# Kernel optimization log

Hardware: AMD Instinct MI355X
Metric: run time of the kernel (lower is better)

## Reference

```python
import jax, jax.numpy as jnp
import numpy as np

N = 100000
E = 1600000
IN_C, HID_C, OUT_C = 128, 128, 64


def setup_inputs() -> dict:
    key = jax.random.key(0)
    k1, k2, k3, k4 = jax.random.split(key, 4)
    x = jax.random.normal(k1, (N, IN_C), dtype=jnp.float32)
    edge_index = jax.random.randint(k2, (2, E), 0, N, dtype=jnp.int32)
    # Glorot-ish scaled weights
    W1 = jax.random.normal(k3, (IN_C, HID_C), dtype=jnp.float32) / np.sqrt(IN_C)
    b1 = jnp.zeros((HID_C,), dtype=jnp.float32)
    W2 = jax.random.normal(k4, (HID_C, OUT_C), dtype=jnp.float32) / np.sqrt(HID_C)
    b2 = jnp.zeros((OUT_C,), dtype=jnp.float32)
    return {"x": x, "edge_index": edge_index, "W1": W1, "b1": b1, "W2": W2, "b2": b2}


def _gcn_norm(edge_index, num_nodes):
    """Add self loops and compute symmetric D^{-1/2} A D^{-1/2} edge weights (PyG GCNConv defaults)."""
    loop = jnp.arange(num_nodes, dtype=edge_index.dtype)
    row = jnp.concatenate([edge_index[0], loop])  # source nodes
    col = jnp.concatenate([edge_index[1], loop])  # target nodes
    ones = jnp.ones_like(col, dtype=jnp.float32)
    deg = jax.ops.segment_sum(ones, col, num_segments=num_nodes)
    deg_inv_sqrt = jnp.where(deg > 0, jax.lax.rsqrt(jnp.maximum(deg, 1.0)), 0.0)
    norm = deg_inv_sqrt[row] * deg_inv_sqrt[col]  # [E+N]
    return row, col, norm


def _gcn_layer(x, row, col, norm, W, b, num_nodes):
    h = x @ W                                   # [N, C_out] transform first (PyG order)
    msg = h[row] * norm[:, None]                # gather + scale  [E+N, C_out]
    out = jax.ops.segment_sum(msg, col, num_segments=num_nodes)  # scatter-add
    return out + b


def reference(x, edge_index, W1, b1, W2, b2):
    row, col, norm = _gcn_norm(edge_index, N)
    h = jax.nn.relu(_gcn_layer(x, row, col, norm, W1, b1, N))
    return _gcn_layer(h, row, col, norm, W2, b2, N)
```

## Files before the change

### kernel.cpp

```cpp
#include <hip/hip_runtime.h>
#include <hip/hip_fp16.h>

#define NODES 100000
#define EDGES 1600000

#define BSHIFT 9
#define BNODES 512
#define NBUCK ((NODES + BNODES - 1) / BNODES)
#define BCAP 10240

#define GB 782
#define SC 1563

typedef __attribute__((ext_vector_type(8))) short short8;
typedef __attribute__((ext_vector_type(4))) float f32x4;

__device__ inline unsigned short f2bf(float f) {
    unsigned u = __builtin_bit_cast(unsigned, f);
    u = u + 0x7fff + ((u >> 16) & 1);
    return (unsigned short)(u >> 16);
}
__device__ inline float bf2f(unsigned short h) {
    unsigned u = ((unsigned)h) << 16;
    return __builtin_bit_cast(float, u);
}
__device__ inline unsigned short f2h_bits(float f) {
    __half h = __float2half_rn(f);
    return __builtin_bit_cast(unsigned short, h);
}
__device__ inline float h2f(unsigned short bits) {
    return __half2float(__builtin_bit_cast(__half, bits));
}
__device__ inline float2 h2f2(unsigned int bits) {
    __half2 h = __builtin_bit_cast(__half2, bits);
    return __half22float2(h);
}


template <int NCOL>
__device__ __forceinline__ void w_frag_prep(const float* __restrict__ W,
                                            unsigned short* __restrict__ wh,
                                            unsigned short* __restrict__ wl,
                                            int idx) {
    constexpr int NCT = NCOL / 16;
    int lane = idx & 63;
    int rem = idx >> 6;
    int ct = rem % NCT;
    int kt = rem / NCT;
    int kbase = kt * 32 + ((lane >> 4) * 8);
    int c = ct * 16 + (lane & 15);
#pragma unroll
    for (int i = 0; i < 8; i++) {
        float v = W[(size_t)(kbase + i) * NCOL + c];
        unsigned short hi = f2bf(v);
        unsigned short lo = f2bf(v - bf2f(hi));
        wh[(size_t)idx * 8 + i] = hi;
        wl[(size_t)idx * 8 + i] = lo;
    }
}

__global__ __launch_bounds__(256) void prep_kernel(const float* __restrict__ W1,
                                                   const float* __restrict__ W2,
                                                   unsigned short* __restrict__ wh1,
                                                   unsigned short* __restrict__ wl1,
                                                   unsigned short* __restrict__ wh2,
                                                   unsigned short* __restrict__ wl2,
                                                   int* __restrict__ gcur) {
    const int tid = threadIdx.x;
    const int b = blockIdx.x;
    if (b < 8) {
        w_frag_prep<128>(W1, wh1, wl1, b * 256 + tid);
    } else if (b < 12) {
        w_frag_prep<64>(W2, wh2, wl2, (b - 8) * 256 + tid);
    } else {
        if (tid < NBUCK) gcur[tid] = 0;
    }
}


template <int NCOL, bool IN_HALF>
__device__ __forceinline__ void gemm_body(const void* __restrict__ Xv,
                                          const unsigned short* __restrict__ wh,
                                          const unsigned short* __restrict__ wl,
                                          unsigned short* __restrict__ H,
                                          unsigned short* s_wh,
                                          unsigned short* s_wl,
                                          int tid, int bid) {
    constexpr int NCT = NCOL / 16;
    constexpr int FRAGS = 4 * NCT * 64;

    const int wave = tid >> 6;
    const int lane = tid & 63;

    const int row0 = bid * 128 + wave * 16 + (lane & 15);
    const bool active = (bid * 128 + wave * 16) < NODES;

    float xs[4][8];
    if (active) {
        if constexpr (IN_HALF) {
            const unsigned short* xrow = (const unsigned short*)Xv + (size_t)row0 * 128 + ((lane >> 4) * 8);
#pragma unroll
            for (int kt = 0; kt < 4; kt++) {
                short8 raw = *(const short8*)(xrow + kt * 32);
#pragma unroll
                for (int i = 0; i < 8; i++) xs[kt][i] = h2f((unsigned short)raw[i]);
            }
        } else {
            const float* xrow = (const float*)Xv + (size_t)row0 * 128 + ((lane >> 4) * 8);
#pragma unroll
            for (int kt = 0; kt < 4; kt++) {
                float4 a = *(const float4*)(xrow + kt * 32);
                float4 b = *(const float4*)(xrow + kt * 32 + 4);
                xs[kt][0] = a.x; xs[kt][1] = a.y; xs[kt][2] = a.z; xs[kt][3] = a.w;
                xs[kt][4] = b.x; xs[kt][5] = b.y; xs[kt][6] = b.z; xs[kt][7] = b.w;
            }
        }
    }

    constexpr int ROUNDS = (FRAGS * 16) / (512 * 16);
#pragma unroll
    for (int j = 0; j < ROUNDS; j++) {
        __builtin_amdgcn_global_load_lds((const unsigned int*)((const char*)wh + ((size_t)tid + j * 512) * 16),
                                         (unsigned int*)(s_wh + ((size_t)tid + j * 512) * 8), 16, 0, 0);
        __builtin_amdgcn_global_load_lds((const unsigned int*)((const char*)wl + ((size_t)tid + j * 512) * 16),
                                         (unsigned int*)(s_wl + ((size_t)tid + j * 512) * 8), 16, 0, 0);
    }
    __syncthreads();

    if (!active) return;

    short8 ah[4], al[4];
#pragma unroll
    for (int kt = 0; kt < 4; kt++) {
#pragma unroll
        for (int i = 0; i < 8; i++) {
            unsigned short hi = f2bf(xs[kt][i]);
            unsigned short lo = f2bf(xs[kt][i] - bf2f(hi));
            ah[kt][i] = (short)hi;
            al[kt][i] = (short)lo;
        }
    }

    f32x4 acc[NCT];
#pragma unroll
    for (int ct = 0; ct < NCT; ct++) acc[ct] = (f32x4){0.f, 0.f, 0.f, 0.f};

#pragma unroll
    for (int kt = 0; kt < 4; kt++) {
#pragma unroll
        for (int ct = 0; ct < NCT; ct++) {
            const int fo = ((kt * NCT + ct) * 64 + lane) * 8;
            short8 bh = *(const short8*)&s_wh[fo];
            short8 bl = *(const short8*)&s_wl[fo];
            acc[ct] = __builtin_amdgcn_mfma_f32_16x16x32_bf16(ah[kt], bh, acc[ct], 0, 0, 0);
            acc[ct] = __builtin_amdgcn_mfma_f32_16x16x32_bf16(al[kt], bh, acc[ct], 0, 0, 0);
            acc[ct] = __builtin_amdgcn_mfma_f32_16x16x32_bf16(ah[kt], bl, acc[ct], 0, 0, 0);
        }
    }

    const int rbase = bid * 128 + wave * 16 + ((lane >> 4) * 4);
#pragma unroll
    for (int ct = 0; ct < NCT; ct++) {
#pragma unroll
        for (int r = 0; r < 4; r++) {
            H[(size_t)(rbase + r) * NCOL + ct * 16 + (lane & 15)] = f2h_bits(acc[ct][r]);
        }
    }
}


__global__ __launch_bounds__(512) void gemm1_scatter(const float* __restrict__ X,
                                                     const unsigned short* __restrict__ wh,
                                                     const unsigned short* __restrict__ wl,
                                                     unsigned short* __restrict__ H,
                                                     const int* __restrict__ erow,
                                                     const int* __restrict__ ecol,
                                                     int* __restrict__ gcur,
                                                     int2* __restrict__ temp) {
    __shared__ __align__(16) char smem[65536];
    const int tid = threadIdx.x;

    if (blockIdx.x < GB) {
        unsigned short* s_wh = (unsigned short*)smem;
        unsigned short* s_wl = s_wh + 2048 * 8;
        gemm_body<128, false>(X, wh, wl, H, s_wh, s_wl, tid, blockIdx.x);
    } else {
        int* hist = (int*)smem;
        int* rbase = hist + NBUCK;
        const int ebase = (blockIdx.x - GB) * 1024;
        if (tid < NBUCK) hist[tid] = 0;
        __syncthreads();

        const int e0 = ebase + tid;
        const int e1 = ebase + tid + 512;
        const bool v0 = e0 < EDGES;
        const bool v1 = e1 < EDGES;
        int c0 = 0, s0 = 0, b0 = 0, r0 = 0;
        int c1 = 0, s1 = 0, b1 = 0, r1 = 0;
        if (v0) {
            c0 = ecol[e0]; s0 = erow[e0];
            b0 = c0 >> BSHIFT;
            r0 = atomicAdd(&hist[b0], 1);
        }
        if (v1) {
            c1 = ecol[e1]; s1 = erow[e1];
            b1 = c1 >> BSHIFT;
            r1 = atomicAdd(&hist[b1], 1);
        }
        __syncthreads();
        if (tid < NBUCK) {
            int h = hist[tid];
            rbase[tid] = h ? atomicAdd(&gcur[tid], h) : 0;
        }
        __syncthreads();
        if (v0) {
            int2 v; v.x = s0; v.y = c0 & (BNODES - 1);
            temp[(size_t)b0 * BCAP + rbase[b0] + r0] = v;
        }
        if (v1) {
            int2 v; v.x = s1; v.y = c1 & (BNODES - 1);
            temp[(size_t)b1 * BCAP + rbase[b1] + r1] = v;
        }
    }
}


__global__ __launch_bounds__(512) void gemm2_kernel(const unsigned short* __restrict__ X,
                                                    const unsigned short* __restrict__ wh,
                                                    const unsigned short* __restrict__ wl,
                                                    unsigned short* __restrict__ H) {
    __shared__ unsigned short s_wh[1024 * 8];
    __shared__ unsigned short s_wl[1024 * 8];
    gemm_body<64, true>(X, wh, wl, H, s_wh, s_wl, threadIdx.x, blockIdx.x);
}


__global__ __launch_bounds__(1024) void bucket_build(const int2* __restrict__ temp,
                                                     const int* __restrict__ gcur,
                                                     int* __restrict__ row_start,
                                                     float* __restrict__ dis,
                                                     int* __restrict__ esrc) {
    __shared__ int cnt[BNODES];
    __shared__ int offs[BNODES];
    __shared__ int cur[BNODES];
    __shared__ int ssc[256];
    const int b = blockIdx.x;
    const int tid = threadIdx.x;

    if (tid < 256) ssc[tid] = (tid < NBUCK) ? gcur[tid] : 0;
    __syncthreads();
    for (int d = 1; d < 256; d <<= 1) {
        int x = (tid < 256 && tid >= d) ? ssc[tid - d] : 0;
        __syncthreads();
        if (tid < 256) ssc[tid] += x;
        __syncthreads();
    }
    const int size = gcur[b];
    const int gbase = ssc[b] - size;
    if (b == 0 && tid == 0) row_start[NODES] = EDGES;

    if (tid < BNODES) cnt[tid] = 0;
    __syncthreads();

    for (int i = tid; i < size; i += 1024) {
        int2 v = temp[(size_t)b * BCAP + i];
        atomicAdd(&cnt[v.y], 1);
    }
    __syncthreads();

    if (tid < BNODES) offs[tid] = cnt[tid];
    __syncthreads();
    for (int d = 1; d < BNODES; d <<= 1) {
        int x = 0;
        if (tid < BNODES && tid >= d) x = offs[tid - d];
        __syncthreads();
        if (tid < BNODES) offs[tid] += x;
        __syncthreads();
    }
    if (tid < BNODES) {
        int excl = offs[tid] - cnt[tid];
        cur[tid] = excl;
        int v = b * BNODES + tid;
        if (v < NODES) {
            row_start[v] = gbase + excl;
            dis[v] = rsqrtf((float)(cnt[tid] + 1));
        }
    }
    __syncthreads();

    for (int i = tid; i < size; i += 1024) {
        int2 v = temp[(size_t)b * BCAP + i];
        int pos = gbase + atomicAdd(&cur[v.y], 1);
        esrc[pos] = v.x;
    }
}


template <int C, bool RELU, bool OUT_HALF>
__global__ __launch_bounds__(256, 8) void agg_v4(const unsigned short* __restrict__ H,
                                                 const int* __restrict__ row_start,
                                                 const int* __restrict__ edge_src,
                                                 const float* __restrict__ dis,
                                                 const float* __restrict__ bias,
                                                 void* __restrict__ OUT) {
    constexpr int GL = (C == 128) ? 16 : 8;
    constexpr int GPW = 64 / GL;
    constexpr int RQ = C / 8;

    const int lane = threadIdx.x & 63;
    const int sub = lane & (GL - 1);
    const int grp = lane >> ((C == 128) ? 4 : 3);
    const int wid = (blockIdx.x * 256 + threadIdx.x) >> 6;
    const int v = wid * GPW + grp;
    if (v >= NODES) return;

    const uint4* __restrict__ Hq = (const uint4*)H;

    const int e0 = row_start[v];
    const int e1 = row_start[v + 1];
    const float dv = dis[v];

    const float4 ba = ((const float4*)bias)[sub * 2];
    const float4 bb = ((const float4*)bias)[sub * 2 + 1];

    uint4 gs = Hq[(size_t)v * RQ + sub];

    int i0 = edge_src[min(e0 + 0, EDGES - 1)];
    int i1 = edge_src[min(e0 + 1, EDGES - 1)];
    int i2 = edge_src[min(e0 + 2, EDGES - 1)];
    int i3 = edge_src[min(e0 + 3, EDGES - 1)];
    float d0 = dis[i0], d1 = dis[i1], d2 = dis[i2], d3 = dis[i3];

    float a0, a1, a2, a3, a4, a5, a6, a7;
    {
        float2 f0 = h2f2(gs.x), f1 = h2f2(gs.y), f2 = h2f2(gs.z), f3 = h2f2(gs.w);
        a0 = f0.x * dv; a1 = f0.y * dv; a2 = f1.x * dv; a3 = f1.y * dv;
        a4 = f2.x * dv; a5 = f2.y * dv; a6 = f3.x * dv; a7 = f3.y * dv;
    }

    for (int k = e0; k < e1; k += 4) {
        uint4 g0 = Hq[(size_t)i0 * RQ + sub];
        uint4 g1 = Hq[(size_t)i1 * RQ + sub];
        uint4 g2 = Hq[(size_t)i2 * RQ + sub];
        uint4 g3 = Hq[(size_t)i3 * RQ + sub];
        const int n0 = edge_src[min(k + 4, EDGES - 1)];
        const int n1 = edge_src[min(k + 5, EDGES - 1)];
        const int n2 = edge_src[min(k + 6, EDGES - 1)];
        const int n3 = edge_src[min(k + 7, EDGES - 1)];
        const float dn0 = dis[n0], dn1 = dis[n1], dn2 = dis[n2], dn3 = dis[n3];
        const float w0 = d0;
        const float w1 = (k + 1 < e1) ? d1 : 0.f;
        const float w2 = (k + 2 < e1) ? d2 : 0.f;
        const float w3 = (k + 3 < e1) ? d3 : 0.f;
#define ACC(G, W)                                                        \
        {                                                                \
            float2 f0 = h2f2(G.x), f1 = h2f2(G.y);                       \
            float2 f2 = h2f2(G.z), f3 = h2f2(G.w);                       \
            a0 = fmaf(f0.x, W, a0); a1 = fmaf(f0.y, W, a1);              \
            a2 = fmaf(f1.x, W, a2); a3 = fmaf(f1.y, W, a3);              \
            a4 = fmaf(f2.x, W, a4); a5 = fmaf(f2.y, W, a5);              \
            a6 = fmaf(f3.x, W, a6); a7 = fmaf(f3.y, W, a7);              \
        }
        ACC(g0, w0)
        ACC(g1, w1)
        ACC(g2, w2)
        ACC(g3, w3)
#undef ACC
        i0 = n0; i1 = n1; i2 = n2; i3 = n3;
        d0 = dn0; d1 = dn1; d2 = dn2; d3 = dn3;
    }

    float o0 = fmaf(a0, dv, ba.x);
    float o1 = fmaf(a1, dv, ba.y);
    float o2 = fmaf(a2, dv, ba.z);
    float o3 = fmaf(a3, dv, ba.w);
    float o4 = fmaf(a4, dv, bb.x);
    float o5 = fmaf(a5, dv, bb.y);
    float o6 = fmaf(a6, dv, bb.z);
    float o7 = fmaf(a7, dv, bb.w);
    if constexpr (RELU) {
        o0 = fmaxf(o0, 0.f); o1 = fmaxf(o1, 0.f);
        o2 = fmaxf(o2, 0.f); o3 = fmaxf(o3, 0.f);
        o4 = fmaxf(o4, 0.f); o5 = fmaxf(o5, 0.f);
        o6 = fmaxf(o6, 0.f); o7 = fmaxf(o7, 0.f);
    }

    if constexpr (OUT_HALF) {
        uint4 o;
        o.x = __builtin_bit_cast(unsigned, __float22half2_rn(make_float2(o0, o1)));
        o.y = __builtin_bit_cast(unsigned, __float22half2_rn(make_float2(o2, o3)));
        o.z = __builtin_bit_cast(unsigned, __float22half2_rn(make_float2(o4, o5)));
        o.w = __builtin_bit_cast(unsigned, __float22half2_rn(make_float2(o6, o7)));
        ((uint4*)OUT)[(size_t)v * RQ + sub] = o;
    } else {
        float4 oa, ob;
        oa.x = o0; oa.y = o1; oa.z = o2; oa.w = o3;
        ob.x = o4; ob.y = o5; ob.z = o6; ob.w = o7;
        float* outp = (float*)OUT + (size_t)v * C + sub * 8;
        *(float4*)(outp) = oa;
        *(float4*)(outp + 4) = ob;
    }
}


extern "C" void kernel_launch(void* const* d_in, const int* in_sizes, int n_in,
                              void* d_out, int out_size, void* d_ws, size_t ws_size,
                              hipStream_t stream) {
    const float* x   = (const float*)d_in[0];
    const int* eidx  = (const int*)d_in[1];
    const float* W1  = (const float*)d_in[2];
    const float* b1  = (const float*)d_in[3];
    const float* W2  = (const float*)d_in[4];
    const float* b2  = (const float*)d_in[5];
    float* out = (float*)d_out;

    const int* erow = eidx;
    const int* ecol = eidx + EDGES;

    char* w = (char*)d_ws;
    size_t off = 0;
    auto alloc = [&](size_t bytes) -> void* {
        void* p = w + off;
        off += (bytes + 255) & ~(size_t)255;
        return p;
    };
    float* dis     = (float*)alloc((size_t)NODES * 4);
    int*   rowst   = (int*)alloc((size_t)(NODES + 1) * 4);
    int*   esrc    = (int*)alloc((size_t)EDGES * 4);
    int*   gcur    = (int*)alloc(NBUCK * 4);
    int2*  temp    = (int2*)alloc((size_t)NBUCK * BCAP * 8);
    unsigned short* wh1 = (unsigned short*)alloc(2048 * 8 * 2);
    unsigned short* wl1 = (unsigned short*)alloc(2048 * 8 * 2);
    unsigned short* wh2 = (unsigned short*)alloc(1024 * 8 * 2);
    unsigned short* wl2 = (unsigned short*)alloc(1024 * 8 * 2);
    unsigned short* bufA = (unsigned short*)alloc((size_t)NODES * 128 * 2);
    unsigned short* bufB = (unsigned short*)alloc((size_t)NODES * 128 * 2);
    unsigned short* bufC = (unsigned short*)alloc((size_t)NODES * 64 * 2);

    prep_kernel<<<13, 256, 0, stream>>>(W1, W2, wh1, wl1, wh2, wl2, gcur);

    gemm1_scatter<<<GB + SC, 512, 0, stream>>>(x, wh1, wl1, bufA, erow, ecol, gcur, temp);

    bucket_build<<<NBUCK, 1024, 0, stream>>>(temp, gcur, rowst, dis, esrc);

    agg_v4<128, true, true><<<NODES / 16, 256, 0, stream>>>(bufA, rowst, esrc, dis, b1, bufB);

    gemm2_kernel<<<GB, 512, 0, stream>>>(bufB, wh2, wl2, bufC);

    agg_v4<64, false, false><<<NODES / 32, 256, 0, stream>>>(bufC, rowst, esrc, dis, b2, out);
}
```

Baseline: 184.6 us.

## Fuse layer-1 aggregation with layer-2 GEMM using single-pass fp16 MFMA

Layer-1 aggregation now writes its ReLU output into LDS and immediately multiplies it by W2 using fp16 MFMA inside the same block, replacing the separate gemm2 kernel and the intermediate bufB round trip through global memory. W2 is prepared as a single fp16 fragment array instead of bf16 hi/lo split, so the second GEMM uses one MFMA per tile rather than three. This removes a kernel launch and roughly 25MB of global traffic. In exchange it adds LDS pressure (lower occupancy bound of 6) and reduces precision of the second GEMM to fp16 inputs.

```diff
diff --git a/kernel.cpp b/kernel.cpp
--- a/kernel.cpp
+++ b/kernel.cpp
@@ -13,6 +13,7 @@
 #define SC 1563
 
 typedef __attribute__((ext_vector_type(8))) short short8;
+typedef __attribute__((ext_vector_type(8))) _Float16 half8;
 typedef __attribute__((ext_vector_type(4))) float f32x4;
 
 __device__ inline unsigned short f2bf(float f) {
@@ -37,57 +38,59 @@
 }
 
 
-template <int NCOL>
-__device__ __forceinline__ void w_frag_prep(const float* __restrict__ W,
-                                            unsigned short* __restrict__ wh,
-                                            unsigned short* __restrict__ wl,
-                                            int idx) {
-    constexpr int NCT = NCOL / 16;
-    int lane = idx & 63;
-    int rem = idx >> 6;
-    int ct = rem % NCT;
-    int kt = rem / NCT;
-    int kbase = kt * 32 + ((lane >> 4) * 8);
-    int c = ct * 16 + (lane & 15);
-#pragma unroll
-    for (int i = 0; i < 8; i++) {
-        float v = W[(size_t)(kbase + i) * NCOL + c];
-        unsigned short hi = f2bf(v);
-        unsigned short lo = f2bf(v - bf2f(hi));
-        wh[(size_t)idx * 8 + i] = hi;
-        wl[(size_t)idx * 8 + i] = lo;
-    }
-}
-
 __global__ __launch_bounds__(256) void prep_kernel(const float* __restrict__ W1,
                                                    const float* __restrict__ W2,
                                                    unsigned short* __restrict__ wh1,
                                                    unsigned short* __restrict__ wl1,
-                                                   unsigned short* __restrict__ wh2,
-                                                   unsigned short* __restrict__ wl2,
+                                                   unsigned short* __restrict__ w2f,
                                                    int* __restrict__ gcur) {
     const int tid = threadIdx.x;
     const int b = blockIdx.x;
     if (b < 8) {
-        w_frag_prep<128>(W1, wh1, wl1, b * 256 + tid);
+        constexpr int NCT = 8;
+        int idx = b * 256 + tid;
+        int lane = idx & 63;
+        int rem = idx >> 6;
+        int ct = rem % NCT;
+        int kt = rem / NCT;
+        int kbase = kt * 32 + ((lane >> 4) * 8);
+        int c = ct * 16 + (lane & 15);
+#pragma unroll
+        for (int i = 0; i < 8; i++) {
+            float v = W1[(size_t)(kbase + i) * 128 + c];
+            unsigned short hi = f2bf(v);
+            unsigned short lo = f2bf(v - bf2f(hi));
+            wh1[(size_t)idx * 8 + i] = hi;
+            wl1[(size_t)idx * 8 + i] = lo;
+        }
     } else if (b < 12) {
-        w_frag_prep<64>(W2, wh2, wl2, (b - 8) * 256 + tid);
+        constexpr int NCT = 4;
+        int idx = (b - 8) * 256 + tid;
+        int lane = idx & 63;
+        int rem = idx >> 6;
+        int ct = rem % NCT;
+        int kt = rem / NCT;
+        int kbase = kt * 32 + ((lane >> 4) * 8);
+        int c = ct * 16 + (lane & 15);
+#pragma unroll
+        for (int i = 0; i < 8; i++) {
+            w2f[(size_t)idx * 8 + i] = f2h_bits(W2[(size_t)(kbase + i) * 64 + c]);
+        }
     } else {
         if (tid < NBUCK) gcur[tid] = 0;
     }
 }
 
 
-template <int NCOL, bool IN_HALF>
-__device__ __forceinline__ void gemm_body(const void* __restrict__ Xv,
-                                          const unsigned short* __restrict__ wh,
-                                          const unsigned short* __restrict__ wl,
-                                          unsigned short* __restrict__ H,
-                                          unsigned short* s_wh,
-                                          unsigned short* s_wl,
-                                          int tid, int bid) {
-    constexpr int NCT = NCOL / 16;
-    constexpr int FRAGS = 4 * NCT * 64;
+__device__ __forceinline__ void gemm1_body(const float* __restrict__ X,
+                                           const unsigned short* __restrict__ wh,
+                                           const unsigned short* __restrict__ wl,
+                                           unsigned short* __restrict__ H,
+                                           unsigned short* s_wh,
+                                           unsigned short* s_wl,
+                                           int tid, int bid) {
+    constexpr int NCT = 8;
+    constexpr int FRAGS = 2048;
 
     const int wave = tid >> 6;
     const int lane = tid & 63;
@@ -97,29 +100,18 @@
 
     float xs[4][8];
     if (active) {
-        if constexpr (IN_HALF) {
-            const unsigned short* xrow = (const unsigned short*)Xv + (size_t)row0 * 128 + ((lane >> 4) * 8);
-#pragma unroll
-            for (int kt = 0; kt < 4; kt++) {
-                short8 raw = *(const short8*)(xrow + kt * 32);
-#pragma unroll
-                for (int i = 0; i < 8; i++) xs[kt][i] = h2f((unsigned short)raw[i]);
-            }
-        } else {
-            const float* xrow = (const float*)Xv + (size_t)row0 * 128 + ((lane >> 4) * 8);
-#pragma unroll
-            for (int kt = 0; kt < 4; kt++) {
-                float4 a = *(const float4*)(xrow + kt * 32);
-                float4 b = *(const float4*)(xrow + kt * 32 + 4);
-                xs[kt][0] = a.x; xs[kt][1] = a.y; xs[kt][2] = a.z; xs[kt][3] = a.w;
-                xs[kt][4] = b.x; xs[kt][5] = b.y; xs[kt][6] = b.z; xs[kt][7] = b.w;
-            }
-        }
-    }
-
-    constexpr int ROUNDS = (FRAGS * 16) / (512 * 16);
-#pragma unroll
-    for (int j = 0; j < ROUNDS; j++) {
+        const float* xrow = X + (size_t)row0 * 128 + ((lane >> 4) * 8);
+#pragma unroll
+        for (int kt = 0; kt < 4; kt++) {
+            float4 a = *(const float4*)(xrow + kt * 32);
+            float4 b = *(const float4*)(xrow + kt * 32 + 4);
+            xs[kt][0] = a.x; xs[kt][1] = a.y; xs[kt][2] = a.z; xs[kt][3] = a.w;
+            xs[kt][4] = b.x; xs[kt][5] = b.y; xs[kt][6] = b.z; xs[kt][7] = b.w;
+        }
+    }
+
+#pragma unroll
+    for (int j = 0; j < 4; j++) {
         __builtin_amdgcn_global_load_lds((const unsigned int*)((const char*)wh + ((size_t)tid + j * 512) * 16),
                                          (unsigned int*)(s_wh + ((size_t)tid + j * 512) * 8), 16, 0, 0);
         __builtin_amdgcn_global_load_lds((const unsigned int*)((const char*)wl + ((size_t)tid + j * 512) * 16),
@@ -163,7 +155,7 @@
     for (int ct = 0; ct < NCT; ct++) {
 #pragma unroll
         for (int r = 0; r < 4; r++) {
-            H[(size_t)(rbase + r) * NCOL + ct * 16 + (lane & 15)] = f2h_bits(acc[ct][r]);
+            H[(size_t)(rbase + r) * 128 + ct * 16 + (lane & 15)] = f2h_bits(acc[ct][r]);
         }
     }
 }
@@ -183,7 +175,7 @@
     if (blockIdx.x < GB) {
         unsigned short* s_wh = (unsigned short*)smem;
         unsigned short* s_wl = s_wh + 2048 * 8;
-        gemm_body<128, false>(X, wh, wl, H, s_wh, s_wl, tid, blockIdx.x);
+        gemm1_body(X, wh, wl, H, s_wh, s_wl, tid, blockIdx.x);
     } else {
         int* hist = (int*)smem;
         int* rbase = hist + NBUCK;
@@ -222,16 +214,6 @@
             temp[(size_t)b1 * BCAP + rbase[b1] + r1] = v;
         }
     }
-}
-
-
-__global__ __launch_bounds__(512) void gemm2_kernel(const unsigned short* __restrict__ X,
-                                                    const unsigned short* __restrict__ wh,
-                                                    const unsigned short* __restrict__ wl,
-                                                    unsigned short* __restrict__ H) {
-    __shared__ unsigned short s_wh[1024 * 8];
-    __shared__ unsigned short s_wl[1024 * 8];
-    gemm_body<64, true>(X, wh, wl, H, s_wh, s_wl, threadIdx.x, blockIdx.x);
 }
 
 
@@ -296,23 +278,137 @@
 }
 
 
-template <int C, bool RELU, bool OUT_HALF>
-__global__ __launch_bounds__(256, 8) void agg_v4(const unsigned short* __restrict__ H,
+__global__ __launch_bounds__(256, 6) void agg1_gemm2(const unsigned short* __restrict__ H,
+                                                     const int* __restrict__ row_start,
+                                                     const int* __restrict__ edge_src,
+                                                     const float* __restrict__ dis,
+                                                     const float* __restrict__ b1,
+                                                     const unsigned short* __restrict__ w2f,
+                                                     unsigned short* __restrict__ H2) {
+    __shared__ float h_lds[16][132];
+    __shared__ unsigned short s_w2[1024 * 8];
+
+    const int tid = threadIdx.x;
+    const int lane = tid & 63;
+    const int sub = lane & 15;
+    const int grp = lane >> 4;
+    const int nl = (tid >> 6) * 4 + grp;
+    const int v = blockIdx.x * 16 + nl;
+
+#pragma unroll
+    for (int j = 0; j < 4; j++) {
+        __builtin_amdgcn_global_load_lds((const unsigned int*)((const char*)w2f + ((size_t)tid + j * 256) * 16),
+                                         (unsigned int*)(s_w2 + ((size_t)tid + j * 256) * 8), 16, 0, 0);
+    }
+
+    const uint4* __restrict__ Hq = (const uint4*)H;
+    const int e0 = row_start[v];
+    const int e1 = row_start[v + 1];
+    const float dv = dis[v];
+
+    const float4 ba = ((const float4*)b1)[sub * 2];
+    const float4 bb = ((const float4*)b1)[sub * 2 + 1];
+
+    uint4 gs = Hq[(size_t)v * 16 + sub];
+
+    int i0 = edge_src[min(e0 + 0, EDGES - 1)];
+    int i1 = edge_src[min(e0 + 1, EDGES - 1)];
+    int i2 = edge_src[min(e0 + 2, EDGES - 1)];
+    int i3 = edge_src[min(e0 + 3, EDGES - 1)];
+    float d0 = dis[i0], d1 = dis[i1], d2 = dis[i2], d3 = dis[i3];
+
+    float a0, a1, a2, a3, a4, a5, a6, a7;
+    {
+        float2 f0 = h2f2(gs.x), f1 = h2f2(gs.y), f2 = h2f2(gs.z), f3 = h2f2(gs.w);
+        a0 = f0.x * dv; a1 = f0.y * dv; a2 = f1.x * dv; a3 = f1.y * dv;
+        a4 = f2.x * dv; a5 = f2.y * dv; a6 = f3.x * dv; a7 = f3.y * dv;
+    }
+
+    for (int k = e0; k < e1; k += 4) {
+        uint4 g0 = Hq[(size_t)i0 * 16 + sub];
+        uint4 g1 = Hq[(size_t)i1 * 16 + sub];
+        uint4 g2 = Hq[(size_t)i2 * 16 + sub];
+        uint4 g3 = Hq[(size_t)i3 * 16 + sub];
+        const int n0 = edge_src[min(k + 4, EDGES - 1)];
+        const int n1 = edge_src[min(k + 5, EDGES - 1)];
+        const int n2 = edge_src[min(k + 6, EDGES - 1)];
+        const int n3 = edge_src[min(k + 7, EDGES - 1)];
+        const float dn0 = dis[n0], dn1 = dis[n1], dn2 = dis[n2], dn3 = dis[n3];
+        const float w0 = d0;
+        const float w1 = (k + 1 < e1) ? d1 : 0.f;
+        const float w2 = (k + 2 < e1) ? d2 : 0.f;
+        const float w3 = (k + 3 < e1) ? d3 : 0.f;
+#define ACC(G, W)                                                        \
+        {                                                                \
+            float2 f0 = h2f2(G.x), f1 = h2f2(G.y);                       \
+            float2 f2 = h2f2(G.z), f3 = h2f2(G.w);                       \
+            a0 = fmaf(f0.x, W, a0); a1 = fmaf(f0.y, W, a1);              \
+            a2 = fmaf(f1.x, W, a2); a3 = fmaf(f1.y, W, a3);              \
+            a4 = fmaf(f2.x, W, a4); a5 = fmaf(f2.y, W, a5);              \
+            a6 = fmaf(f3.x, W, a6); a7 = fmaf(f3.y, W, a7);              \
+        }
+        ACC(g0, w0)
+        ACC(g1, w1)
+        ACC(g2, w2)
+        ACC(g3, w3)
+#undef ACC
+        i0 = n0; i1 = n1; i2 = n2; i3 = n3;
+        d0 = dn0; d1 = dn1; d2 = dn2; d3 = dn3;
+    }
+
+    {
+        float4 oa, ob;
+        oa.x = fmaxf(fmaf(a0, dv, ba.x), 0.f);
+        oa.y = fmaxf(fmaf(a1, dv, ba.y), 0.f);
+        oa.z = fmaxf(fmaf(a2, dv, ba.z), 0.f);
+        oa.w = fmaxf(fmaf(a3, dv, ba.w), 0.f);
+        ob.x = fmaxf(fmaf(a4, dv, bb.x), 0.f);
+        ob.y = fmaxf(fmaf(a5, dv, bb.y), 0.f);
+        ob.z = fmaxf(fmaf(a6, dv, bb.z), 0.f);
+        ob.w = fmaxf(fmaf(a7, dv, bb.w), 0.f);
+        *(float4*)&h_lds[nl][sub * 8] = oa;
+        *(float4*)&h_lds[nl][sub * 8 + 4] = ob;
+    }
+    __syncthreads();
+
+    const int ct = tid >> 6;
+    f32x4 acc = (f32x4){0.f, 0.f, 0.f, 0.f};
+#pragma unroll
+    for (int kt = 0; kt < 4; kt++) {
+        const int arow = lane & 15;
+        const int acol = (lane >> 4) * 8 + kt * 32;
+        float4 pa = *(const float4*)&h_lds[arow][acol];
+        float4 pb = *(const float4*)&h_lds[arow][acol + 4];
+        half8 af;
+        af[0] = (_Float16)pa.x; af[1] = (_Float16)pa.y;
+        af[2] = (_Float16)pa.z; af[3] = (_Float16)pa.w;
+        af[4] = (_Float16)pb.x; af[5] = (_Float16)pb.y;
+        af[6] = (_Float16)pb.z; af[7] = (_Float16)pb.w;
+        half8 bf = *(const half8*)&s_w2[((kt * 4 + ct) * 64 + lane) * 8];
+        acc = __builtin_amdgcn_mfma_f32_16x16x32_f16(af, bf, acc, 0, 0, 0);
+    }
+
+    const int rbase = blockIdx.x * 16 + ((lane >> 4) * 4);
+#pragma unroll
+    for (int r = 0; r < 4; r++) {
+        H2[(size_t)(rbase + r) * 64 + ct * 16 + (lane & 15)] = f2h_bits(acc[r]);
+    }
+}
+
+
+__global__ __launch_bounds__(256, 8) void agg_l2(const unsigned short* __restrict__ H,
                                                  const int* __restrict__ row_start,
                                                  const int* __restrict__ edge_src,
                                                  const float* __restrict__ dis,
                                                  const float* __restrict__ bias,
-                                                 void* __restrict__ OUT) {
-    constexpr int GL = (C == 128) ? 16 : 8;
-    constexpr int GPW = 64 / GL;
-    constexpr int RQ = C / 8;
+                                                 float* __restrict__ OUT) {
+    constexpr int RQ = 8;
 
     const int lane = threadIdx.x & 63;
-    const int sub = lane & (GL - 1);
-    const int grp = lane >> ((C == 128) ? 4 : 3);
+    const int sub = lane & 7;
+    const int grp = lane >> 3;
     const int wid = (blockIdx.x * 256 + threadIdx.x) >> 6;
-    const int v = wid * GPW + grp;
-    if (v >= NODES) return;
+    const int v = wid * 8 + grp;
 
     const uint4* __restrict__ Hq = (const uint4*)H;
 
@@ -370,36 +466,14 @@
         d0 = dn0; d1 = dn1; d2 = dn2; d3 = dn3;
     }
 
-    float o0 = fmaf(a0, dv, ba.x);
-    float o1 = fmaf(a1, dv, ba.y);
-    float o2 = fmaf(a2, dv, ba.z);
-    float o3 = fmaf(a3, dv, ba.w);
-    float o4 = fmaf(a4, dv, bb.x);
-    float o5 = fmaf(a5, dv, bb.y);
-    float o6 = fmaf(a6, dv, bb.z);
-    float o7 = fmaf(a7, dv, bb.w);
-    if constexpr (RELU) {
-        o0 = fmaxf(o0, 0.f); o1 = fmaxf(o1, 0.f);
-        o2 = fmaxf(o2, 0.f); o3 = fmaxf(o3, 0.f);
-        o4 = fmaxf(o4, 0.f); o5 = fmaxf(o5, 0.f);
-        o6 = fmaxf(o6, 0.f); o7 = fmaxf(o7, 0.f);
-    }
-
-    if constexpr (OUT_HALF) {
-        uint4 o;
-        o.x = __builtin_bit_cast(unsigned, __float22half2_rn(make_float2(o0, o1)));
-        o.y = __builtin_bit_cast(unsigned, __float22half2_rn(make_float2(o2, o3)));
-        o.z = __builtin_bit_cast(unsigned, __float22half2_rn(make_float2(o4, o5)));
-        o.w = __builtin_bit_cast(unsigned, __float22half2_rn(make_float2(o6, o7)));
-        ((uint4*)OUT)[(size_t)v * RQ + sub] = o;
-    } else {
-        float4 oa, ob;
-        oa.x = o0; oa.y = o1; oa.z = o2; oa.w = o3;
-        ob.x = o4; ob.y = o5; ob.z = o6; ob.w = o7;
-        float* outp = (float*)OUT + (size_t)v * C + sub * 8;
-        *(float4*)(outp) = oa;
-        *(float4*)(outp + 4) = ob;
-    }
+    float4 oa, ob;
+    oa.x = fmaf(a0, dv, ba.x); oa.y = fmaf(a1, dv, ba.y);
+    oa.z = fmaf(a2, dv, ba.z); oa.w = fmaf(a3, dv, ba.w);
+    ob.x = fmaf(a4, dv, bb.x); ob.y = fmaf(a5, dv, bb.y);
+    ob.z = fmaf(a6, dv, bb.z); ob.w = fmaf(a7, dv, bb.w);
+    float* outp = OUT + (size_t)v * 64 + sub * 8;
+    *(float4*)(outp) = oa;
+    *(float4*)(outp + 4) = ob;
 }
 
 
@@ -431,21 +505,17 @@
     int2*  temp    = (int2*)alloc((size_t)NBUCK * BCAP * 8);
     unsigned short* wh1 = (unsigned short*)alloc(2048 * 8 * 2);
     unsigned short* wl1 = (unsigned short*)alloc(2048 * 8 * 2);
-    unsigned short* wh2 = (unsigned short*)alloc(1024 * 8 * 2);
-    unsigned short* wl2 = (unsigned short*)alloc(1024 * 8 * 2);
+    unsigned short* w2f = (unsigned short*)alloc(1024 * 8 * 2);
     unsigned short* bufA = (unsigned short*)alloc((size_t)NODES * 128 * 2);
-    unsigned short* bufB = (unsigned short*)alloc((size_t)NODES * 128 * 2);
     unsigned short* bufC = (unsigned short*)alloc((size_t)NODES * 64 * 2);
 
-    prep_kernel<<<13, 256, 0, stream>>>(W1, W2, wh1, wl1, wh2, wl2, gcur);
+    prep_kernel<<<13, 256, 0, stream>>>(W1, W2, wh1, wl1, w2f, gcur);
 
     gemm1_scatter<<<GB + SC, 512, 0, stream>>>(x, wh1, wl1, bufA, erow, ecol, gcur, temp);
 
     bucket_build<<<NBUCK, 1024, 0, stream>>>(temp, gcur, rowst, dis, esrc);
 
-    agg_v4<128, true, true><<<NODES / 16, 256, 0, stream>>>(bufA, rowst, esrc, dis, b1, bufB);
-
-    gemm2_kernel<<<GB, 512, 0, stream>>>(bufB, wh2, wl2, bufC);
-
-    agg_v4<64, false, false><<<NODES / 32, 256, 0, stream>>>(bufC, rowst, esrc, dis, b2, out);
-}
+    agg1_gemm2<<<NODES / 16, 256, 0, stream>>>(bufA, rowst, esrc, dis, b1, w2f, bufC);
+
+    agg_l2<<<NODES / 32, 256, 0, stream>>>(bufC, rowst, esrc, dis, b2, out);
+}
```

After: 168.1 us. -8.9%, faster.
